# Performance work log

Hardware: AMD Instinct MI355X
Metric: run time of the kernel (lower is better)

## Reference

```python
import jax, jax.numpy as jnp
import numpy as np

B, N, D = 4, 2048, 1024
H = 16
DH = D // H


def setup_inputs() -> dict:
    key = jax.random.key(0)
    ks = jax.random.split(key, 9)
    s_in = 1.0 / np.sqrt(D)
    x = jax.random.normal(ks[0], (B, N, D), dtype=jnp.float32)
    Wq = jax.random.uniform(ks[1], (D, D), jnp.float32, -s_in, s_in)
    bq = jax.random.uniform(ks[2], (D,), jnp.float32, -s_in, s_in)
    Wk = jax.random.uniform(ks[3], (D, D), jnp.float32, -s_in, s_in)
    bk = jax.random.uniform(ks[4], (D,), jnp.float32, -s_in, s_in)
    Wv = jax.random.uniform(ks[5], (D, D), jnp.float32, -s_in, s_in)
    bv = jax.random.uniform(ks[6], (D,), jnp.float32, -s_in, s_in)
    Wo = jax.random.uniform(ks[7], (D, D), jnp.float32, -s_in, s_in)
    bo = jax.random.uniform(ks[8], (D,), jnp.float32, -s_in, s_in)
    return {"x": x, "Wq": Wq, "bq": bq, "Wk": Wk, "bk": bk,
            "Wv": Wv, "bv": bv, "Wo": Wo, "bo": bo}


def reference(x, Wq, bq, Wk, bk, Wv, bv, Wo, bo):
    b, n, d = x.shape
    q = (x @ Wq + bq).reshape(b, n, H, DH)  # (b, n, h, dh)
    k = (x @ Wk + bk).reshape(b, n, H, DH)
    v = (x @ Wv + bv).reshape(b, n, H, DH)
    scale = 1.0 / jnp.sqrt(jnp.asarray(DH, x.dtype))
    scores = jnp.einsum("bqhd,bkhd->bhqk", q, k) * scale  # (b, h, n, n)
    # valid = arange(1..n) per query => causal mask: key index < valid[q] = q+1
    causal = jnp.arange(n)[None, :] <= jnp.arange(n)[:, None]  # (n_q, n_k)
    scores = jnp.where(causal[None, None, :, :], scores, -jnp.inf)
    weights = jax.nn.softmax(scores, axis=-1)
    out = jnp.einsum("bhqk,bkhd->bqhd", weights, v).reshape(b, n, d)
    return out @ Wo + bo
```

## Files before the change

### kernel.cpp

```cpp
#include <hip/hip_runtime.h>
#include <hip/hip_bf16.h>
#include <math.h>

namespace {
constexpr int B_ = 4, N_ = 2048, D_ = 1024, H_ = 16, DH_ = 64;
constexpr int M_ = B_ * N_;
}

typedef __bf16 bf16x8 __attribute__((ext_vector_type(8)));
typedef __bf16 bf16x4 __attribute__((ext_vector_type(4)));
typedef float  f32x4  __attribute__((ext_vector_type(4)));

__device__ inline void async_copy16(const void* g, void* l) {
    __builtin_amdgcn_global_load_lds(
        (const __attribute__((address_space(1))) unsigned int*)g,
        (__attribute__((address_space(3))) unsigned int*)l, 16, 0, 0);
}

__device__ inline float fast_exp2(float x) {
#if __has_builtin(__builtin_amdgcn_exp2f)
    return __builtin_amdgcn_exp2f(x);
#else
    return exp2f(x);
#endif
}

__device__ inline int swz(int row, int c) {
    return c ^ (row & 3) ^ ((row >> 2) & 3);
}

__global__ __launch_bounds__(256) void cast_x(
        const float* __restrict__ x, __bf16* __restrict__ xb)
{
    const size_t i = ((size_t)blockIdx.x * 256 + threadIdx.x) * 8;
    const float4 a = *reinterpret_cast<const float4*>(x + i);
    const float4 b = *reinterpret_cast<const float4*>(x + i + 4);
    bf16x8 o;
    o[0] = (__bf16)a.x; o[1] = (__bf16)a.y; o[2] = (__bf16)a.z; o[3] = (__bf16)a.w;
    o[4] = (__bf16)b.x; o[5] = (__bf16)b.y; o[6] = (__bf16)b.z; o[7] = (__bf16)b.w;
    *reinterpret_cast<bf16x8*>(xb + i) = o;
}

__global__ __launch_bounds__(256) void cast_w(
        const float* __restrict__ Wq, const float* __restrict__ Wk,
        const float* __restrict__ Wv, const float* __restrict__ Wo,
        __bf16* __restrict__ wqkvt, __bf16* __restrict__ wot)
{
    __shared__ float t[64][65];
    const int z = blockIdx.z;
    const float* W = (z == 0) ? Wq : (z == 1) ? Wk : (z == 2) ? Wv : Wo;
    __bf16* dst = (z < 3) ? (wqkvt + (size_t)z * D_ * D_) : wot;
    const int k0 = blockIdx.x * 64, n0 = blockIdx.y * 64;
    const int tid = threadIdx.x;
    #pragma unroll
    for (int p = 0; p < 16; ++p) {
        const int idx = p * 256 + tid;
        const int r = idx >> 6, c = idx & 63;
        t[r][c] = W[(size_t)(k0 + r) * D_ + n0 + c];
    }
    __syncthreads();
    #pragma unroll
    for (int p = 0; p < 16; ++p) {
        const int idx = p * 256 + tid;
        const int r = idx >> 6, c = idx & 63;
        dst[(size_t)(n0 + r) * D_ + k0 + c] = (__bf16)t[c][r];
    }
}

__global__ __launch_bounds__(256) void qkv_mfma(
        const __bf16* __restrict__ A, const __bf16* __restrict__ Bt,
        const float* __restrict__ bq, const float* __restrict__ bk,
        const float* __restrict__ bv,
        __bf16* __restrict__ qo, __bf16* __restrict__ ko, __bf16* __restrict__ vo)
{
    __shared__ __align__(16) __bf16 As[128 * 32];
    __shared__ __align__(16) __bf16 Bs[128 * 32];
    const int tid = threadIdx.x;
    const int w = tid >> 6, lane = tid & 63;
    const int l15 = lane & 15, quad = lane >> 4;
    const int tm = blockIdx.x * 128;
    const int tn = blockIdx.y * 128;

    f32x4 acc[4][4] = {};

    for (int k0 = 0; k0 < D_; k0 += 32) {
        __syncthreads();
        #pragma unroll
        for (int it = 0; it < 2; ++it) {
            const int c = it * 256 + tid;
            const int r = c >> 2, pc = c & 3;
            const int lc = swz(r, pc);
            async_copy16(A + (size_t)(tm + r) * D_ + k0 + lc * 8, As + c * 8);
            async_copy16(Bt + (size_t)(tn + r) * D_ + k0 + lc * 8, Bs + c * 8);
        }
        __syncthreads();

        bf16x8 af[4], bfr[4];
        #pragma unroll
        for (int t = 0; t < 4; ++t) {
            const int row = (w >> 1) * 64 + t * 16 + l15;
            af[t] = *reinterpret_cast<const bf16x8*>(
                As + (row * 4 + swz(row, quad)) * 8);
            const int col = (w & 1) * 64 + t * 16 + l15;
            bfr[t] = *reinterpret_cast<const bf16x8*>(
                Bs + (col * 4 + swz(col, quad)) * 8);
        }
        #pragma unroll
        for (int mt = 0; mt < 4; ++mt)
            #pragma unroll
            for (int nt = 0; nt < 4; ++nt)
                acc[mt][nt] = __builtin_amdgcn_mfma_f32_16x16x32_bf16(
                    af[mt], bfr[nt], acc[mt][nt], 0, 0, 0);
    }

    const int z = blockIdx.y >> 3;
    const float* bias = (z == 0) ? bq : (z == 1) ? bk : bv;
    const int col0 = (blockIdx.y & 7) * 128 + (w & 1) * 64;
    const int h = col0 >> 6;
    float bcol[4];
    #pragma unroll
    for (int nt = 0; nt < 4; ++nt) bcol[nt] = bias[col0 + nt * 16 + l15];
    const int gr0 = tm + (w >> 1) * 64;

    if (z < 2) {
        __bf16* dst = (z == 0) ? qo : ko;
        const float sc = (z == 0) ? 0.125f * 1.44269504f : 1.0f;
        #pragma unroll
        for (int mt = 0; mt < 4; ++mt)
            #pragma unroll
            for (int i = 0; i < 4; ++i) {
                const int gr = gr0 + mt * 16 + quad * 4 + i;
                const int b = gr >> 11, tok = gr & (N_ - 1);
                __bf16* row = dst + ((size_t)(b * H_ + h) * N_ + tok) * DH_;
                #pragma unroll
                for (int nt = 0; nt < 4; ++nt)
                    row[nt * 16 + l15] = (__bf16)((acc[mt][nt][i] + bcol[nt]) * sc);
            }
    } else {
        #pragma unroll
        for (int mt = 0; mt < 4; ++mt) {
            const int gr = gr0 + mt * 16 + quad * 4;
            const int b = gr >> 11, tok = gr & (N_ - 1);
            #pragma unroll
            for (int nt = 0; nt < 4; ++nt) {
                const int dh = nt * 16 + l15;
                bf16x4 pv;
                #pragma unroll
                for (int i = 0; i < 4; ++i)
                    pv[i] = (__bf16)(acc[mt][nt][i] + bcol[nt]);
                *reinterpret_cast<bf16x4*>(
                    vo + ((size_t)(b * H_ + h) * DH_ + dh) * N_ + tok) = pv;
            }
        }
    }
}

__global__ __launch_bounds__(256) void out_mfma(
        const __bf16* __restrict__ A, const __bf16* __restrict__ Bt,
        const float* __restrict__ bias, float* __restrict__ out)
{
    __shared__ __align__(16) __bf16 As[128 * 32];
    __shared__ __align__(16) __bf16 Bs[128 * 32];
    const int tid = threadIdx.x;
    const int w = tid >> 6, lane = tid & 63;
    const int l15 = lane & 15, quad = lane >> 4;
    const int tm = blockIdx.x * 128;
    const int tn = blockIdx.y * 128;

    f32x4 acc[4][4] = {};

    for (int k0 = 0; k0 < D_; k0 += 32) {
        __syncthreads();
        #pragma unroll
        for (int it = 0; it < 2; ++it) {
            const int c = it * 256 + tid;
            const int r = c >> 2, pc = c & 3;
            const int lc = swz(r, pc);
            async_copy16(A + (size_t)(tm + r) * D_ + k0 + lc * 8, As + c * 8);
            async_copy16(Bt + (size_t)(tn + r) * D_ + k0 + lc * 8, Bs + c * 8);
        }
        __syncthreads();

        bf16x8 af[4], bfr[4];
        #pragma unroll
        for (int t = 0; t < 4; ++t) {
            const int row = (w >> 1) * 64 + t * 16 + l15;
            af[t] = *reinterpret_cast<const bf16x8*>(
                As + (row * 4 + swz(row, quad)) * 8);
            const int col = (w & 1) * 64 + t * 16 + l15;
            bfr[t] = *reinterpret_cast<const bf16x8*>(
                Bs + (col * 4 + swz(col, quad)) * 8);
        }
        #pragma unroll
        for (int mt = 0; mt < 4; ++mt)
            #pragma unroll
            for (int nt = 0; nt < 4; ++nt)
                acc[mt][nt] = __builtin_amdgcn_mfma_f32_16x16x32_bf16(
                    af[mt], bfr[nt], acc[mt][nt], 0, 0, 0);
    }

    const int col0 = tn + (w & 1) * 64;
    float bcol[4];
    #pragma unroll
    for (int nt = 0; nt < 4; ++nt) bcol[nt] = bias[col0 + nt * 16 + l15];
    const int gr0 = tm + (w >> 1) * 64;
    #pragma unroll
    for (int mt = 0; mt < 4; ++mt)
        #pragma unroll
        for (int i = 0; i < 4; ++i) {
            const int gr = gr0 + mt * 16 + quad * 4 + i;
            float* row = out + (size_t)gr * D_;
            #pragma unroll
            for (int nt = 0; nt < 4; ++nt)
                row[col0 + nt * 16 + l15] = acc[mt][nt][i] + bcol[nt];
        }
}

__global__ __launch_bounds__(256, 4) void attn(
        const __bf16* __restrict__ Q, const __bf16* __restrict__ K,
        const __bf16* __restrict__ Vt, __bf16* __restrict__ ctx)
{
    const int blk = blockIdx.x;
    const int bh = blk & 63;
    const int qb = ((blk >> 6) + bh) & 15;
    const int tid = threadIdx.x;
    const int w = tid >> 6, lane = tid & 63;
    const int l15 = lane & 15, quad = lane >> 4;
    const int qt0 = qb * 128;

    __shared__ __align__(16) __bf16 Ks[64 * 64];
    __shared__ __align__(16) __bf16 Vs[64 * 64];
    __shared__ __align__(16) __bf16 Ps[4][2][16 * 72];

    bf16x8 bqf[2][2];
    #pragma unroll
    for (int qc = 0; qc < 2; ++qc) {
        const size_t base = ((size_t)bh * N_ + qt0 + w * 32 + qc * 16 + l15) * DH_;
        bqf[qc][0] = *reinterpret_cast<const bf16x8*>(Q + base + quad * 8);
        bqf[qc][1] = *reinterpret_cast<const bf16x8*>(Q + base + 32 + quad * 8);
    }

    f32x4 acc[2][4] = {};
    float l_lane[2] = {0.f, 0.f};

    const __bf16* Kg = K + (size_t)bh * N_ * DH_;
    const __bf16* Vg = Vt + (size_t)bh * DH_ * N_;
    const int nkb = 2 * qb + 2;
    const int sr = lane >> 3;
    const int sc = lane & 7;

    for (int kb = 0; kb < nkb; ++kb) {
        __syncthreads();
        #pragma unroll
        for (int j = 0; j < 2; ++j) {
            const int r = j * 32 + w * 8 + sr;
            const int cl = sc ^ (r & 7);
            async_copy16(Kg + (size_t)(kb * 64 + r) * DH_ + cl * 8,
                         &Ks[(j * 256 + tid) * 8]);
            async_copy16(Vg + (size_t)r * N_ + kb * 64 + cl * 8,
                         &Vs[(j * 256 + tid) * 8]);
        }
        __syncthreads();

        f32x4 st[2][4];
        __builtin_amdgcn_s_setprio(1);
        #pragma unroll
        for (int ct = 0; ct < 4; ++ct) {
            const int row = ct * 16 + l15;
            const bf16x8 ka0 = *reinterpret_cast<const bf16x8*>(
                &Ks[(row * 8 + (quad ^ (row & 7))) * 8]);
            const bf16x8 ka1 = *reinterpret_cast<const bf16x8*>(
                &Ks[(row * 8 + ((quad + 4) ^ (row & 7))) * 8]);
            #pragma unroll
            for (int qc = 0; qc < 2; ++qc) {
                f32x4 t = {};
                t = __builtin_amdgcn_mfma_f32_16x16x32_bf16(ka0, bqf[qc][0], t, 0, 0, 0);
                t = __builtin_amdgcn_mfma_f32_16x16x32_bf16(ka1, bqf[qc][1], t, 0, 0, 0);
                st[qc][ct] = t;
            }
        }
        __builtin_amdgcn_s_setprio(0);
        if (kb >= 2 * qb) {
            #pragma unroll
            for (int qc = 0; qc < 2; ++qc) {
                const int q_glob = qt0 + w * 32 + qc * 16 + l15;
                #pragma unroll
                for (int ct = 0; ct < 4; ++ct)
                    #pragma unroll
                    for (int i = 0; i < 4; ++i) {
                        const int k_glob = kb * 64 + ct * 16 + quad * 4 + i;
                        if (k_glob > q_glob) st[qc][ct][i] = -INFINITY;
                    }
            }
        }

        #pragma unroll
        for (int qc = 0; qc < 2; ++qc) {
            float rs = 0.f;
            #pragma unroll
            for (int ct = 0; ct < 4; ++ct) {
                bf16x4 pk;
                #pragma unroll
                for (int i = 0; i < 4; ++i) {
                    const float p = fast_exp2(st[qc][ct][i]);
                    rs += p;
                    pk[i] = (__bf16)p;
                }
                *reinterpret_cast<bf16x4*>(
                    &Ps[w][qc][l15 * 72 + ct * 16 + quad * 4]) = pk;
            }
            l_lane[qc] += rs;
        }

        bf16x8 pa0[2], pa1[2];
        #pragma unroll
        for (int qc = 0; qc < 2; ++qc) {
            pa0[qc] = *reinterpret_cast<const bf16x8*>(
                &Ps[w][qc][l15 * 72 + quad * 8]);
            pa1[qc] = *reinterpret_cast<const bf16x8*>(
                &Ps[w][qc][l15 * 72 + 32 + quad * 8]);
        }
        __builtin_amdgcn_s_setprio(1);
        #pragma unroll
        for (int ct = 0; ct < 4; ++ct) {
            const int row = ct * 16 + l15;
            const bf16x8 vb0 = *reinterpret_cast<const bf16x8*>(
                &Vs[(row * 8 + (quad ^ (row & 7))) * 8]);
            const bf16x8 vb1 = *reinterpret_cast<const bf16x8*>(
                &Vs[(row * 8 + ((quad + 4) ^ (row & 7))) * 8]);
            #pragma unroll
            for (int qc = 0; qc < 2; ++qc) {
                f32x4 t = acc[qc][ct];
                t = __builtin_amdgcn_mfma_f32_16x16x32_bf16(pa0[qc], vb0, t, 0, 0, 0);
                t = __builtin_amdgcn_mfma_f32_16x16x32_bf16(pa1[qc], vb1, t, 0, 0, 0);
                acc[qc][ct] = t;
            }
        }
        __builtin_amdgcn_s_setprio(0);
    }

    const int b = bh >> 4, h = bh & 15;
    #pragma unroll
    for (int qc = 0; qc < 2; ++qc) {
        float r = l_lane[qc];
        r += __shfl_xor(r, 16);
        r += __shfl_xor(r, 32);
        const float linv = 1.0f / r;
        float lT[4];
        #pragma unroll
        for (int i = 0; i < 4; ++i) lT[i] = __shfl(linv, quad * 4 + i);
        #pragma unroll
        for (int i = 0; i < 4; ++i) {
            const int row = qt0 + w * 32 + qc * 16 + quad * 4 + i;
            __bf16* dst = ctx + ((size_t)b * N_ + row) * D_ + h * DH_;
            #pragma unroll
            for (int ct = 0; ct < 4; ++ct)
                dst[ct * 16 + l15] = (__bf16)(acc[qc][ct][i] * lT[i]);
        }
    }
}

extern "C" void kernel_launch(void* const* d_in, const int* in_sizes, int n_in,
                              void* d_out, int out_size, void* d_ws, size_t ws_size,
                              hipStream_t stream) {
    const float* x  = (const float*)d_in[0];
    const float* Wq = (const float*)d_in[1];
    const float* bq = (const float*)d_in[2];
    const float* Wk = (const float*)d_in[3];
    const float* bk = (const float*)d_in[4];
    const float* Wv = (const float*)d_in[5];
    const float* bv = (const float*)d_in[6];
    const float* Wo = (const float*)d_in[7];
    const float* bo = (const float*)d_in[8];
    float* out = (float*)d_out;

    __bf16* xb    = (__bf16*)d_ws;
    __bf16* wqkvt = xb + (size_t)M_ * D_;
    __bf16* wot   = wqkvt + (size_t)3 * D_ * D_;
    __bf16* q     = wot + (size_t)D_ * D_;
    __bf16* k     = q + (size_t)M_ * D_;
    __bf16* vt    = k + (size_t)M_ * D_;
    __bf16* ctx   = vt + (size_t)M_ * D_;

    cast_x<<<dim3(M_ * D_ / (256 * 8)), 256, 0, stream>>>(x, xb);
    cast_w<<<dim3(16, 16, 4), 256, 0, stream>>>(Wq, Wk, Wv, Wo, wqkvt, wot);
    qkv_mfma<<<dim3(M_ / 128, 3 * D_ / 128), 256, 0, stream>>>(
        xb, wqkvt, bq, bk, bv, q, k, vt);
    attn<<<dim3(1024), 256, 0, stream>>>(q, k, vt, ctx);
    out_mfma<<<dim3(M_ / 128, D_ / 128), 256, 0, stream>>>(ctx, wot, bo, out);
}
```

Before: 248.8 us.

## Rewrite QKV GEMM with 256x256 tiles, BK=64 and double-buffered async loads

Rebuilds the QKV projection GEMM around 512-thread blocks computing 256x256 tiles with a K step of 64. The LDS is double-buffered so async global-to-LDS loads for step t+2 overlap MFMA work on the current buffer, synchronised with vmcnt waits. It also uses an XOR swizzle over 8 chunks and raises wave priority around the MFMA bursts. The goal is more operand reuse per tile and hidden load latency. The cost is 128KB of LDS per block and a grid of only 384 blocks, which may leave CUs underoccupied.

```diff
diff --git a/kernel.cpp b/kernel.cpp
--- a/kernel.cpp
+++ b/kernel.cpp
@@ -67,87 +67,136 @@
     }
 }
 
-__global__ __launch_bounds__(256) void qkv_mfma(
+__global__ __launch_bounds__(512, 2) void qkv_mfma(
         const __bf16* __restrict__ A, const __bf16* __restrict__ Bt,
         const float* __restrict__ bq, const float* __restrict__ bk,
         const float* __restrict__ bv,
         __bf16* __restrict__ qo, __bf16* __restrict__ ko, __bf16* __restrict__ vo)
 {
-    __shared__ __align__(16) __bf16 As[128 * 32];
-    __shared__ __align__(16) __bf16 Bs[128 * 32];
+    __shared__ __align__(16) __bf16 As[2][256 * 64];
+    __shared__ __align__(16) __bf16 Bs[2][256 * 64];
     const int tid = threadIdx.x;
     const int w = tid >> 6, lane = tid & 63;
     const int l15 = lane & 15, quad = lane >> 4;
-    const int tm = blockIdx.x * 128;
-    const int tn = blockIdx.y * 128;
-
-    f32x4 acc[4][4] = {};
-
-    for (int k0 = 0; k0 < D_; k0 += 32) {
-        __syncthreads();
-        #pragma unroll
-        for (int it = 0; it < 2; ++it) {
-            const int c = it * 256 + tid;
-            const int r = c >> 2, pc = c & 3;
-            const int lc = swz(r, pc);
-            async_copy16(A + (size_t)(tm + r) * D_ + k0 + lc * 8, As + c * 8);
-            async_copy16(Bt + (size_t)(tn + r) * D_ + k0 + lc * 8, Bs + c * 8);
-        }
-        __syncthreads();
-
-        bf16x8 af[4], bfr[4];
-        #pragma unroll
-        for (int t = 0; t < 4; ++t) {
-            const int row = (w >> 1) * 64 + t * 16 + l15;
-            af[t] = *reinterpret_cast<const bf16x8*>(
-                As + (row * 4 + swz(row, quad)) * 8);
-            const int col = (w & 1) * 64 + t * 16 + l15;
-            bfr[t] = *reinterpret_cast<const bf16x8*>(
-                Bs + (col * 4 + swz(col, quad)) * 8);
-        }
-        #pragma unroll
-        for (int mt = 0; mt < 4; ++mt)
-            #pragma unroll
-            for (int nt = 0; nt < 4; ++nt)
-                acc[mt][nt] = __builtin_amdgcn_mfma_f32_16x16x32_bf16(
-                    af[mt], bfr[nt], acc[mt][nt], 0, 0, 0);
-    }
-
-    const int z = blockIdx.y >> 3;
+    const int wr = w >> 2, wc = w & 3;
+    const int tm = blockIdx.x * 256;
+    const int bn = blockIdx.y * 256;
+
+    const __bf16* Ag = A + (size_t)tm * D_;
+    const __bf16* Bg = Bt + (size_t)bn * D_;
+
+    f32x4 acc[8][4] = {};
+
+    auto stage = [&](int t) {
+        const int k0 = t * 64;
+        __bf16* Ad = As[t & 1];
+        __bf16* Bd = Bs[t & 1];
+        #pragma unroll
+        for (int s = 0; s < 4; ++s) {
+            const int idx = s * 512 + tid;
+            const int r = idx >> 3, cs = idx & 7;
+            const int cl = cs ^ (r & 7);
+            async_copy16(Ag + (size_t)r * D_ + k0 + cl * 8, Ad + idx * 8);
+        }
+        #pragma unroll
+        for (int s = 0; s < 4; ++s) {
+            const int idx = s * 512 + tid;
+            const int r = idx >> 3, cs = idx & 7;
+            const int cl = cs ^ (r & 7);
+            async_copy16(Bg + (size_t)r * D_ + k0 + cl * 8, Bd + idx * 8);
+        }
+    };
+
+    stage(0);
+    stage(1);
+    asm volatile("s_waitcnt vmcnt(8)" ::: "memory");
+    __builtin_amdgcn_s_barrier();
+    __builtin_amdgcn_sched_barrier(0);
+
+    for (int t = 0; t < 16; ++t) {
+        const __bf16* Ab = As[t & 1];
+        const __bf16* Bb = Bs[t & 1];
+        #pragma unroll
+        for (int q = 0; q < 4; ++q) {
+            const int ar0 = wr * 128 + (q >> 1) * 64;
+            const int bc0 = wc * 64 + (q & 1) * 32;
+            bf16x8 af[4][2], bf[2][2];
+            #pragma unroll
+            for (int fr = 0; fr < 4; ++fr) {
+                const int row = ar0 + fr * 16 + l15;
+                #pragma unroll
+                for (int ks = 0; ks < 2; ++ks)
+                    af[fr][ks] = *reinterpret_cast<const bf16x8*>(
+                        Ab + row * 64 + ((ks * 4 + quad) ^ (row & 7)) * 8);
+            }
+            #pragma unroll
+            for (int nc = 0; nc < 2; ++nc) {
+                const int col = bc0 + nc * 16 + l15;
+                #pragma unroll
+                for (int ks = 0; ks < 2; ++ks)
+                    bf[nc][ks] = *reinterpret_cast<const bf16x8*>(
+                        Bb + col * 64 + ((ks * 4 + quad) ^ (col & 7)) * 8);
+            }
+            __builtin_amdgcn_s_setprio(1);
+            #pragma unroll
+            for (int fr = 0; fr < 4; ++fr)
+                #pragma unroll
+                for (int nc = 0; nc < 2; ++nc) {
+                    f32x4 c = acc[(q >> 1) * 4 + fr][(q & 1) * 2 + nc];
+                    c = __builtin_amdgcn_mfma_f32_16x16x32_bf16(af[fr][0], bf[nc][0], c, 0, 0, 0);
+                    c = __builtin_amdgcn_mfma_f32_16x16x32_bf16(af[fr][1], bf[nc][1], c, 0, 0, 0);
+                    acc[(q >> 1) * 4 + fr][(q & 1) * 2 + nc] = c;
+                }
+            __builtin_amdgcn_s_setprio(0);
+            __builtin_amdgcn_s_barrier();
+        }
+        if (t < 14) {
+            stage(t + 2);
+            asm volatile("s_waitcnt vmcnt(8)" ::: "memory");
+        } else if (t == 14) {
+            asm volatile("s_waitcnt vmcnt(0)" ::: "memory");
+        }
+        if (t < 15) {
+            __builtin_amdgcn_s_barrier();
+            __builtin_amdgcn_sched_barrier(0);
+        }
+    }
+
+    const int z = blockIdx.y >> 2;
     const float* bias = (z == 0) ? bq : (z == 1) ? bk : bv;
-    const int col0 = (blockIdx.y & 7) * 128 + (w & 1) * 64;
-    const int h = col0 >> 6;
+    const int ysec = blockIdx.y & 3;
+    const int h = ysec * 4 + wc;
     float bcol[4];
     #pragma unroll
-    for (int nt = 0; nt < 4; ++nt) bcol[nt] = bias[col0 + nt * 16 + l15];
-    const int gr0 = tm + (w >> 1) * 64;
+    for (int nc = 0; nc < 4; ++nc) bcol[nc] = bias[h * 64 + nc * 16 + l15];
+    const int gr0 = tm + wr * 128;
 
     if (z < 2) {
         __bf16* dst = (z == 0) ? qo : ko;
         const float sc = (z == 0) ? 0.125f * 1.44269504f : 1.0f;
         #pragma unroll
-        for (int mt = 0; mt < 4; ++mt)
+        for (int mr = 0; mr < 8; ++mr)
             #pragma unroll
             for (int i = 0; i < 4; ++i) {
-                const int gr = gr0 + mt * 16 + quad * 4 + i;
+                const int gr = gr0 + mr * 16 + quad * 4 + i;
                 const int b = gr >> 11, tok = gr & (N_ - 1);
                 __bf16* row = dst + ((size_t)(b * H_ + h) * N_ + tok) * DH_;
                 #pragma unroll
-                for (int nt = 0; nt < 4; ++nt)
-                    row[nt * 16 + l15] = (__bf16)((acc[mt][nt][i] + bcol[nt]) * sc);
+                for (int nc = 0; nc < 4; ++nc)
+                    row[nc * 16 + l15] = (__bf16)((acc[mr][nc][i] + bcol[nc]) * sc);
             }
     } else {
         #pragma unroll
-        for (int mt = 0; mt < 4; ++mt) {
-            const int gr = gr0 + mt * 16 + quad * 4;
+        for (int mr = 0; mr < 8; ++mr) {
+            const int gr = gr0 + mr * 16 + quad * 4;
             const int b = gr >> 11, tok = gr & (N_ - 1);
             #pragma unroll
-            for (int nt = 0; nt < 4; ++nt) {
-                const int dh = nt * 16 + l15;
+            for (int nc = 0; nc < 4; ++nc) {
+                const int dh = nc * 16 + l15;
                 bf16x4 pv;
                 #pragma unroll
                 for (int i = 0; i < 4; ++i)
-                    pv[i] = (__bf16)(acc[mt][nt][i] + bcol[nt]);
+                    pv[i] = (__bf16)(acc[mr][nc][i] + bcol[nc]);
                 *reinterpret_cast<bf16x4*>(
                     vo + ((size_t)(b * H_ + h) * DH_ + dh) * N_ + tok) = pv;
             }
@@ -384,7 +433,7 @@
 
     cast_x<<<dim3(M_ * D_ / (256 * 8)), 256, 0, stream>>>(x, xb);
     cast_w<<<dim3(16, 16, 4), 256, 0, stream>>>(Wq, Wk, Wv, Wo, wqkvt, wot);
-    qkv_mfma<<<dim3(M_ / 128, 3 * D_ / 128), 256, 0, stream>>>(
+    qkv_mfma<<<dim3(M_ / 256, 3 * D_ / 256), 512, 0, stream>>>(
         xb, wqkvt, bq, bk, bv, q, k, vt);
     attn<<<dim3(1024), 256, 0, stream>>>(q, k, vt, ctx);
     out_mfma<<<dim3(M_ / 128, D_ / 128), 256, 0, stream>>>(ctx, wot, bo, out);
```

Result: slower. 267.4 us (+7.5%).

## Double-buffer K/V tiles in attention and merge cast kernels into one launch

Applied to the files above, without the earlier changes.

The attention kernel now keeps two LDS slots for K and V tiles and prefetches the next tile asynchronously while computing on the current one. This replaces the two barriers per iteration with one wait-and-barrier at the end of each iteration. The goal is to hide global-load latency behind MFMA work. Doubling K/V LDS roughly doubles that kernel's shared memory, so the launch-bounds occupancy hint drops from 4 to 3 blocks. The separate x and weight cast kernels are also fused into a single launch to save one kernel launch.

```diff
diff --git a/kernel.cpp b/kernel.cpp
--- a/kernel.cpp
+++ b/kernel.cpp
@@ -29,41 +29,42 @@
     return c ^ (row & 3) ^ ((row >> 2) & 3);
 }
 
-__global__ __launch_bounds__(256) void cast_x(
-        const float* __restrict__ x, __bf16* __restrict__ xb)
-{
-    const size_t i = ((size_t)blockIdx.x * 256 + threadIdx.x) * 8;
-    const float4 a = *reinterpret_cast<const float4*>(x + i);
-    const float4 b = *reinterpret_cast<const float4*>(x + i + 4);
-    bf16x8 o;
-    o[0] = (__bf16)a.x; o[1] = (__bf16)a.y; o[2] = (__bf16)a.z; o[3] = (__bf16)a.w;
-    o[4] = (__bf16)b.x; o[5] = (__bf16)b.y; o[6] = (__bf16)b.z; o[7] = (__bf16)b.w;
-    *reinterpret_cast<bf16x8*>(xb + i) = o;
-}
-
-__global__ __launch_bounds__(256) void cast_w(
+__global__ __launch_bounds__(256) void cast_xw(
+        const float* __restrict__ x, __bf16* __restrict__ xb,
         const float* __restrict__ Wq, const float* __restrict__ Wk,
         const float* __restrict__ Wv, const float* __restrict__ Wo,
         __bf16* __restrict__ wqkvt, __bf16* __restrict__ wot)
 {
     __shared__ float t[64][65];
-    const int z = blockIdx.z;
-    const float* W = (z == 0) ? Wq : (z == 1) ? Wk : (z == 2) ? Wv : Wo;
-    __bf16* dst = (z < 3) ? (wqkvt + (size_t)z * D_ * D_) : wot;
-    const int k0 = blockIdx.x * 64, n0 = blockIdx.y * 64;
+    const int bid = blockIdx.x;
     const int tid = threadIdx.x;
-    #pragma unroll
-    for (int p = 0; p < 16; ++p) {
-        const int idx = p * 256 + tid;
-        const int r = idx >> 6, c = idx & 63;
-        t[r][c] = W[(size_t)(k0 + r) * D_ + n0 + c];
-    }
-    __syncthreads();
-    #pragma unroll
-    for (int p = 0; p < 16; ++p) {
-        const int idx = p * 256 + tid;
-        const int r = idx >> 6, c = idx & 63;
-        dst[(size_t)(n0 + r) * D_ + k0 + c] = (__bf16)t[c][r];
+    if (bid < 4096) {
+        const size_t i = ((size_t)bid * 256 + tid) * 8;
+        const float4 a = *reinterpret_cast<const float4*>(x + i);
+        const float4 b = *reinterpret_cast<const float4*>(x + i + 4);
+        bf16x8 o;
+        o[0] = (__bf16)a.x; o[1] = (__bf16)a.y; o[2] = (__bf16)a.z; o[3] = (__bf16)a.w;
+        o[4] = (__bf16)b.x; o[5] = (__bf16)b.y; o[6] = (__bf16)b.z; o[7] = (__bf16)b.w;
+        *reinterpret_cast<bf16x8*>(xb + i) = o;
+    } else {
+        const int b2 = bid - 4096;
+        const int bx = b2 & 15, by = (b2 >> 4) & 15, z = b2 >> 8;
+        const float* W = (z == 0) ? Wq : (z == 1) ? Wk : (z == 2) ? Wv : Wo;
+        __bf16* dst = (z < 3) ? (wqkvt + (size_t)z * D_ * D_) : wot;
+        const int k0 = bx * 64, n0 = by * 64;
+        #pragma unroll
+        for (int p = 0; p < 16; ++p) {
+            const int idx = p * 256 + tid;
+            const int r = idx >> 6, c = idx & 63;
+            t[r][c] = W[(size_t)(k0 + r) * D_ + n0 + c];
+        }
+        __syncthreads();
+        #pragma unroll
+        for (int p = 0; p < 16; ++p) {
+            const int idx = p * 256 + tid;
+            const int r = idx >> 6, c = idx & 63;
+            dst[(size_t)(n0 + r) * D_ + k0 + c] = (__bf16)t[c][r];
+        }
     }
 }
 
@@ -216,7 +217,7 @@
         }
 }
 
-__global__ __launch_bounds__(256, 4) void attn(
+__global__ __launch_bounds__(256, 3) void attn(
         const __bf16* __restrict__ Q, const __bf16* __restrict__ K,
         const __bf16* __restrict__ Vt, __bf16* __restrict__ ctx)
 {
@@ -228,8 +229,8 @@
     const int l15 = lane & 15, quad = lane >> 4;
     const int qt0 = qb * 128;
 
-    __shared__ __align__(16) __bf16 Ks[64 * 64];
-    __shared__ __align__(16) __bf16 Vs[64 * 64];
+    __shared__ __align__(16) __bf16 Ks[2][64 * 64];
+    __shared__ __align__(16) __bf16 Vs[2][64 * 64];
     __shared__ __align__(16) __bf16 Ps[4][2][16 * 72];
 
     bf16x8 bqf[2][2];
@@ -249,18 +250,28 @@
     const int sr = lane >> 3;
     const int sc = lane & 7;
 
-    for (int kb = 0; kb < nkb; ++kb) {
-        __syncthreads();
+    auto stage = [&](int kb) {
+        const int sl = kb & 1;
         #pragma unroll
         for (int j = 0; j < 2; ++j) {
             const int r = j * 32 + w * 8 + sr;
             const int cl = sc ^ (r & 7);
             async_copy16(Kg + (size_t)(kb * 64 + r) * DH_ + cl * 8,
-                         &Ks[(j * 256 + tid) * 8]);
+                         &Ks[sl][(j * 256 + tid) * 8]);
             async_copy16(Vg + (size_t)r * N_ + kb * 64 + cl * 8,
-                         &Vs[(j * 256 + tid) * 8]);
-        }
-        __syncthreads();
+                         &Vs[sl][(j * 256 + tid) * 8]);
+        }
+    };
+
+    stage(0);
+    asm volatile("s_waitcnt vmcnt(0)" ::: "memory");
+    __builtin_amdgcn_s_barrier();
+
+    for (int kb = 0; kb < nkb; ++kb) {
+        const int sl = kb & 1;
+        if (kb + 1 < nkb) stage(kb + 1);
+        const __bf16* Ksl = Ks[sl];
+        const __bf16* Vsl = Vs[sl];
 
         f32x4 st[2][4];
         __builtin_amdgcn_s_setprio(1);
@@ -268,9 +279,9 @@
         for (int ct = 0; ct < 4; ++ct) {
             const int row = ct * 16 + l15;
             const bf16x8 ka0 = *reinterpret_cast<const bf16x8*>(
-                &Ks[(row * 8 + (quad ^ (row & 7))) * 8]);
+                &Ksl[(row * 8 + (quad ^ (row & 7))) * 8]);
             const bf16x8 ka1 = *reinterpret_cast<const bf16x8*>(
-                &Ks[(row * 8 + ((quad + 4) ^ (row & 7))) * 8]);
+                &Ksl[(row * 8 + ((quad + 4) ^ (row & 7))) * 8]);
             #pragma unroll
             for (int qc = 0; qc < 2; ++qc) {
                 f32x4 t = {};
@@ -325,9 +336,9 @@
         for (int ct = 0; ct < 4; ++ct) {
             const int row = ct * 16 + l15;
             const bf16x8 vb0 = *reinterpret_cast<const bf16x8*>(
-                &Vs[(row * 8 + (quad ^ (row & 7))) * 8]);
+                &Vsl[(row * 8 + (quad ^ (row & 7))) * 8]);
             const bf16x8 vb1 = *reinterpret_cast<const bf16x8*>(
-                &Vs[(row * 8 + ((quad + 4) ^ (row & 7))) * 8]);
+                &Vsl[(row * 8 + ((quad + 4) ^ (row & 7))) * 8]);
             #pragma unroll
             for (int qc = 0; qc < 2; ++qc) {
                 f32x4 t = acc[qc][ct];
@@ -337,6 +348,9 @@
             }
         }
         __builtin_amdgcn_s_setprio(0);
+
+        asm volatile("s_waitcnt vmcnt(0)" ::: "memory");
+        __builtin_amdgcn_s_barrier();
     }
 
     const int b = bh >> 4, h = bh & 15;
@@ -382,8 +396,8 @@
     __bf16* vt    = k + (size_t)M_ * D_;
     __bf16* ctx   = vt + (size_t)M_ * D_;
 
-    cast_x<<<dim3(M_ * D_ / (256 * 8)), 256, 0, stream>>>(x, xb);
-    cast_w<<<dim3(16, 16, 4), 256, 0, stream>>>(Wq, Wk, Wv, Wo, wqkvt, wot);
+    cast_xw<<<dim3(4096 + 1024), 256, 0, stream>>>(
+        x, xb, Wq, Wk, Wv, Wo, wqkvt, wot);
     qkv_mfma<<<dim3(M_ / 128, 3 * D_ / 128), 256, 0, stream>>>(
         xb, wqkvt, bq, bk, bv, q, k, vt);
     attn<<<dim3(1024), 256, 0, stream>>>(q, k, vt, ctx);
```

New measurement: 257.1 us. +3.3%, slower.
